# Kernel tuning notes

Measured on AMD Instinct MI355X. Metric: run time of the kernel, lower is better.

The kernel has to match this reference:

```python
import jax, jax.numpy as jnp
import numpy as np

HID = 2048
N_HEADS = 16
N_KV = 16
HEAD_DIM = HID // N_HEADS
N_EXP = 8
TOP_K = 2
MOE_I = 1408
SH_I = 5632
EPS = 1e-6
ROPE_THETA = 1e6


def _rms(x, w):
    v = jnp.mean(jnp.square(x), axis=-1, keepdims=True)
    return (x * jax.lax.rsqrt(v + EPS)) * w


def _rope(q, k):
    # q, k: [B, S, H, D]
    S, D = q.shape[1], q.shape[-1]
    inv = 1.0 / (ROPE_THETA ** (jnp.arange(0, D, 2, dtype=jnp.float32) / D))
    freqs = jnp.arange(S, dtype=jnp.float32)[:, None] * inv[None, :]   # [S, D/2]
    emb = jnp.concatenate([freqs, freqs], axis=-1)                      # [S, D]
    cos = jnp.cos(emb)[None, :, None, :]
    sin = jnp.sin(emb)[None, :, None, :]
    def rot(t):
        t1, t2 = t[..., : D // 2], t[..., D // 2:]
        return jnp.concatenate([-t2, t1], axis=-1)
    return q * cos + rot(q) * sin, k * cos + rot(k) * sin


def setup_inputs() -> dict:
    key = jax.random.key(0)
    ks = jax.random.split(key, 20)
    s = 0.02
    d = {
        "x": jax.random.normal(ks[0], (2, 1024, HID), jnp.float32),
        "w_ln1": jnp.ones((HID,), jnp.float32),
        "wq": jax.random.normal(ks[1], (HID, N_HEADS * HEAD_DIM), jnp.float32) * s,
        "bq": jnp.zeros((N_HEADS * HEAD_DIM,), jnp.float32),
        "wk": jax.random.normal(ks[2], (HID, N_KV * HEAD_DIM), jnp.float32) * s,
        "bk": jnp.zeros((N_KV * HEAD_DIM,), jnp.float32),
        "wv": jax.random.normal(ks[3], (HID, N_KV * HEAD_DIM), jnp.float32) * s,
        "bv": jnp.zeros((N_KV * HEAD_DIM,), jnp.float32),
        "wo": jax.random.normal(ks[4], (N_HEADS * HEAD_DIM, HID), jnp.float32) * s,
        "w_ln2": jnp.ones((HID,), jnp.float32),
        "w_router": jax.random.normal(ks[5], (HID, N_EXP), jnp.float32) * s,
        "w_gate_e": jax.random.normal(ks[6], (N_EXP, HID, MOE_I), jnp.float32) * s,
        "w_up_e": jax.random.normal(ks[7], (N_EXP, HID, MOE_I), jnp.float32) * s,
        "w_down_e": jax.random.normal(ks[8], (N_EXP, MOE_I, HID), jnp.float32) * s,
        "w_sh_gate": jax.random.normal(ks[9], (HID, SH_I), jnp.float32) * s,
        "w_sh_up": jax.random.normal(ks[10], (HID, SH_I), jnp.float32) * s,
        "w_sh_down": jax.random.normal(ks[11], (SH_I, HID), jnp.float32) * s,
        "w_sh_eg": jax.random.normal(ks[12], (HID, 1), jnp.float32) * s,
    }
    return d


def reference(x, w_ln1, wq, bq, wk, bk, wv, bv, wo, w_ln2, w_router,
              w_gate_e, w_up_e, w_down_e, w_sh_gate, w_sh_up, w_sh_down, w_sh_eg):
    B, S, H = x.shape
    # ---- self-attention (pre-norm) ----
    h = _rms(x, w_ln1)
    q = (h @ wq + bq).reshape(B, S, N_HEADS, HEAD_DIM)
    k = (h @ wk + bk).reshape(B, S, N_KV, HEAD_DIM)
    v = (h @ wv + bv).reshape(B, S, N_KV, HEAD_DIM)
    q, k = _rope(q, k)
    rep = N_HEADS // N_KV
    if rep > 1:
        k = jnp.repeat(k, rep, axis=2)
        v = jnp.repeat(v, rep, axis=2)
    scores = jnp.einsum("bqhd,bkhd->bhqk", q, k) * (HEAD_DIM ** -0.5)
    causal = jnp.tril(jnp.ones((S, S), bool))
    scores = jnp.where(causal[None, None], scores, jnp.finfo(scores.dtype).min)
    attn = jax.nn.softmax(scores, axis=-1)
    ctx = jnp.einsum("bhqk,bkhd->bqhd", attn, v).reshape(B, S, N_HEADS * HEAD_DIM)
    x = x + ctx @ wo

    # ---- sparse MoE FFN (pre-norm) ----
    h = _rms(x, w_ln2).reshape(B * S, H)                     # [T, H]
    logits = h @ w_router                                     # [T, E]
    probs = jax.nn.softmax(logits, axis=-1)
    top_w, top_i = jax.lax.top_k(probs, TOP_K)               # norm_topk_prob=False
    combine = jnp.sum(jax.nn.one_hot(top_i, N_EXP, dtype=h.dtype)
                      * top_w[..., None], axis=1)            # [T, E]
    # dense per-expert compute combined with routing weights (same math as
    # the sorted grouped-GEMM dispatch in Qwen2MoeMLPStack)
    g = jnp.einsum("th,ehi->eti", h, w_gate_e)               # [E, T, I]
    u = jnp.einsum("th,ehi->eti", h, w_up_e)
    y = jnp.einsum("eti,eih->eth", jax.nn.silu(g) * u, w_down_e)
    routed = jnp.einsum("eth,te->th", y, combine)            # [T, H]
    # shared expert with sigmoid gate
    sh = (jax.nn.silu(h @ w_sh_gate) * (h @ w_sh_up)) @ w_sh_down
    sh = sh * jax.nn.sigmoid(h @ w_sh_eg)
    x = x + (routed + sh).reshape(B, S, H)
    return x
```

## Files before the change

### kernel.cpp

```cpp
#include <hip/hip_runtime.h>
#include <hip/hip_bf16.h>
#include <math.h>

#define TOKENS 2048
#define HIDDEN 2048
#define NH 16
#define HD 128
#define SEQ 1024
#define MOE_I 1408
#define SH_I 5632
#define K3 6144
#define MAXROWS 5120

typedef __hip_bfloat16 bf16;
typedef short bf16x8 __attribute__((ext_vector_type(8)));
typedef short bf16x4 __attribute__((ext_vector_type(4)));
typedef float f32x4 __attribute__((ext_vector_type(4)));
typedef float f32x16 __attribute__((ext_vector_type(16)));

__device__ __forceinline__ float b2f(bf16 x) { return __bfloat162float(x); }
__device__ __forceinline__ bf16 f2b(float x) { return __float2bfloat16(x); }
__device__ __forceinline__ void split2(float v, short& hi, short& lo) {
    bf16 h = f2b(v);
    bf16 l = f2b(v - b2f(h));
    hi = __builtin_bit_cast(short, h); lo = __builtin_bit_cast(short, l);
}

__device__ __forceinline__ void load_lds16(const void* g, void* l) {
    __builtin_amdgcn_global_load_lds(
        (const __attribute__((address_space(1))) unsigned int*)g,
        (__attribute__((address_space(3))) unsigned int*)l, 16, 0, 0);
}

__global__ __launch_bounds__(256) void rmsnorm3_k(
    const float* __restrict__ x, const float* __restrict__ w, bf16* __restrict__ out)
{
    const int row = blockIdx.x, tid = threadIdx.x;
    const float4* xr = (const float4*)(x + (size_t)row * HIDDEN);
    float4 v1 = xr[tid], v2 = xr[tid + 256];
    float ss = v1.x*v1.x + v1.y*v1.y + v1.z*v1.z + v1.w*v1.w
             + v2.x*v2.x + v2.y*v2.y + v2.z*v2.z + v2.w*v2.w;
    #pragma unroll
    for (int off = 1; off < 64; off <<= 1) ss += __shfl_xor(ss, off);
    __shared__ float ps[4];
    if ((tid & 63) == 0) ps[tid >> 6] = ss;
    __syncthreads();
    float tot = ps[0] + ps[1] + ps[2] + ps[3];
    float r = rsqrtf(tot * (1.0f / HIDDEN) + 1e-6f);
    bf16* o = out + (size_t)row * 4096;
    float vv[8] = {v1.x, v1.y, v1.z, v1.w, v2.x, v2.y, v2.z, v2.w};
    int idx[8]  = {tid*4, tid*4+1, tid*4+2, tid*4+3,
                   1024+tid*4, 1024+tid*4+1, 1024+tid*4+2, 1024+tid*4+3};
    #pragma unroll
    for (int u = 0; u < 8; u++) {
        short hi, lo; split2(vv[u] * r * w[idx[u]], hi, lo);
        o[idx[u]]        = __builtin_bit_cast(bf16, hi);
        o[2048 + idx[u]] = __builtin_bit_cast(bf16, lo);
    }
}

__global__ __launch_bounds__(256) void transpose_wz(
    const float* __restrict__ W, bf16* __restrict__ Wt, int K, int N,
    int nOff, long zsrc, long zdst)
{
    __shared__ float t[32][33];
    W  += (size_t)blockIdx.z * zsrc;
    Wt += (size_t)blockIdx.z * zdst;
    const int n0 = blockIdx.x * 32, k0 = blockIdx.y * 32;
    const int tx = threadIdx.x & 31, ty = threadIdx.x >> 5;
    #pragma unroll
    for (int i = 0; i < 4; i++)
        t[ty + i*8][tx] = W[(size_t)(k0 + ty + i*8) * N + n0 + tx];
    __syncthreads();
    #pragma unroll
    for (int i = 0; i < 4; i++)
        Wt[(size_t)(nOff + n0 + ty + i*8) * K + k0 + tx] = f2b(t[tx][ty + i*8]);
}

__global__ __launch_bounds__(256) void transpose_w3(
    const float* __restrict__ W, bf16* __restrict__ Wt2, int K, int N, int nOff)
{
    __shared__ float t[32][33];
    const int n0 = blockIdx.x * 32, k0 = blockIdx.y * 32;
    const int tx = threadIdx.x & 31, ty = threadIdx.x >> 5;
    #pragma unroll
    for (int i = 0; i < 4; i++)
        t[ty + i*8][tx] = W[(size_t)(k0 + ty + i*8) * N + n0 + tx];
    __syncthreads();
    #pragma unroll
    for (int i = 0; i < 4; i++) {
        float v = t[tx][ty + i*8];
        short hi, lo; split2(v, hi, lo);
        bf16* o = Wt2 + (size_t)(nOff + n0 + ty + i*8) * (2*K) + k0 + tx;
        o[0] = __builtin_bit_cast(bf16, hi);
        o[K] = __builtin_bit_cast(bf16, lo);
    }
}

__global__ __launch_bounds__(256) void gemm_bt(
    const bf16* __restrict__ A, const bf16* __restrict__ Bt,
    float* __restrict__ Cf, bf16* __restrict__ Cb, const float* __restrict__ bias,
    int M, int N, int K, int ldA, int ldB, int ldC, long zCstride, int limb3, int epi)
{
    __shared__ __align__(16) bf16 As[128 * 64];
    __shared__ __align__(16) bf16 Bs[128 * 64];
    const int tid = threadIdx.x;
    const int lane = tid & 63, wid = tid >> 6;
    const int l32 = lane & 31, lh2 = lane >> 5;
    const int wr = wid >> 1, wc = wid & 1;
    int lid = blockIdx.y * gridDim.x + blockIdx.x;
    {
        const int nwg = gridDim.x * gridDim.y;
        const int q = nwg >> 3, r = nwg & 7;
        const int xcd = lid & 7, idx = lid >> 3;
        lid = (xcd < r ? xcd * (q + 1) : r * (q + 1) + (xcd - r) * q) + idx;
    }
    const int m0 = (lid % gridDim.x) * 128, n0 = (lid / gridDim.x) * 128;
    const int koff = blockIdx.z * K;

    int srow[4], sslot[4];
    #pragma unroll
    for (int i = 0; i < 4; i++) {
        const int c = tid + 256*i;
        srow[i]  = c >> 3;
        sslot[i] = (((c & 7) ^ (srow[i] & 7)) << 3);
    }

    f32x16 acc[2][2];
    #pragma unroll
    for (int m = 0; m < 2; m++)
        #pragma unroll
        for (int n = 0; n < 2; n++)
            #pragma unroll
            for (int j = 0; j < 16; j++) acc[m][n][j] = 0.f;

    for (int k0 = 0; k0 < K; k0 += 64) {
        const int kcat = koff + k0;
        int ka = kcat, kb = kcat;
        if (limb3) {
            ka = (kcat >= 4096) ? kcat - 4096 : kcat;
            kb = (kcat >= 2048) ? kcat - 2048 : kcat;
        }
        __syncthreads();
        #pragma unroll
        for (int i = 0; i < 4; i++) {
            load_lds16(A  + (size_t)(m0 + srow[i]) * ldA + ka + sslot[i], As + (tid + 256*i) * 8);
            load_lds16(Bt + (size_t)(n0 + srow[i]) * ldB + kb + sslot[i], Bs + (tid + 256*i) * 8);
        }
        __syncthreads();
        bf16x8 a[2][4], b[2][4];
        #pragma unroll
        for (int m = 0; m < 2; m++) {
            const int r = wr*64 + m*32 + l32, rx = r & 7;
            #pragma unroll
            for (int kk = 0; kk < 4; kk++)
                a[m][kk] = *(const bf16x8*)&As[r*64 + ((((kk<<1)|lh2) ^ rx) << 3)];
        }
        #pragma unroll
        for (int n = 0; n < 2; n++) {
            const int r = wc*64 + n*32 + l32, rx = r & 7;
            #pragma unroll
            for (int kk = 0; kk < 4; kk++)
                b[n][kk] = *(const bf16x8*)&Bs[r*64 + ((((kk<<1)|lh2) ^ rx) << 3)];
        }
        #pragma unroll
        for (int kk = 0; kk < 4; kk++)
            #pragma unroll
            for (int m = 0; m < 2; m++)
                #pragma unroll
                for (int n = 0; n < 2; n++)
                    acc[m][n] = __builtin_amdgcn_mfma_f32_32x32x16_bf16(a[m][kk], b[n][kk], acc[m][n], 0, 0, 0);
    }

    float* Cz = Cf + (size_t)blockIdx.z * zCstride;
    #pragma unroll
    for (int m = 0; m < 2; m++) {
        const int base_m = m0 + wr*64 + m*32 + 4*lh2;
        #pragma unroll
        for (int n = 0; n < 2; n++) {
// ... 148 lines not shown
        #pragma unroll
        for (int n = 0; n < 2; n++) {
            const int r = wc*64 + n*32 + l32, rx = r & 7;
            #pragma unroll
            for (int kk = 0; kk < 4; kk++)
                b[n][kk] = *(const bf16x8*)&Bs[r*64 + ((((kk<<1)|lh2) ^ rx) << 3)];
        }
        #pragma unroll
        for (int kk = 0; kk < 4; kk++)
            #pragma unroll
            for (int m = 0; m < 2; m++)
                #pragma unroll
                for (int n = 0; n < 2; n++)
                    acc[m][n] = __builtin_amdgcn_mfma_f32_32x32x16_bf16(a[m][kk], b[n][kk], acc[m][n], 0, 0, 0);
    }

    #pragma unroll
    for (int m = 0; m < 2; m++) {
        const int base_m = m0 + wr*64 + m*32 + 4*lh2;
        #pragma unroll
        for (int n = 0; n < 2; n++) {
            const int gcol = n0 + wc*64 + n*32 + l32;
            #pragma unroll
            for (int reg = 0; reg < 16; reg++) {
                const int grow = base_m + (reg & 3) + 8*(reg >> 2);
                Y[(size_t)(off + grow) * 2048 + gcol] = f2b(acc[m][n][reg]);
            }
        }
    }
}

__global__ void rope_table_k(float2* __restrict__ cs)
{
    const int i = blockIdx.x * 256 + threadIdx.x;
    const int s = i >> 6, d = i & 63;
    const float fr = (float)s * powf(1.0e6f, -(float)d * (1.0f / 64.0f));
    float c, sn;
    sincosf(fr, &sn, &c);
    cs[i] = make_float2(c, sn);
}

__global__ void rope_f32_k(float* __restrict__ qkv, const float2* __restrict__ cs)
{
    const int idx = blockIdx.x * 256 + threadIdx.x;
    const int d  = idx & 63;
    const int hh = (idx >> 6) & 15;
    const size_t base = (size_t)(idx >> 10) * 6144 + hh * HD;
    const int s = (idx >> 10) & 1023;
    const float2 t = cs[(s << 6) | d];
    const float c = t.x, sn = t.y;
    float q0 = qkv[base + d], q1 = qkv[base + d + 64];
    qkv[base + d]      = q0 * c - q1 * sn;
    qkv[base + d + 64] = q1 * c + q0 * sn;
    float k0 = qkv[base + 2048 + d], k1 = qkv[base + 2048 + d + 64];
    qkv[base + 2048 + d]      = k0 * c - k1 * sn;
    qkv[base + 2048 + d + 64] = k1 * c + k0 * sn;
}

__global__ __launch_bounds__(256) void transpose_v3_k(
    const float* __restrict__ qkv, bf16* __restrict__ vth, bf16* __restrict__ vtl)
{
    __shared__ float t[32][33];
    const int s0 = blockIdx.x * 32, d0 = blockIdx.y * 32;
    const int bh = blockIdx.z, b = bh >> 4, h = bh & 15;
    const int tx = threadIdx.x & 31, ty = threadIdx.x >> 5;
    const float* vb = qkv + ((size_t)b * SEQ) * 6144 + 4096 + h * HD;
    #pragma unroll
    for (int i = 0; i < 4; i++)
        t[ty + i*8][tx] = vb[(size_t)(s0 + ty + i*8) * 6144 + d0 + tx];
    __syncthreads();
    const size_t ob = ((size_t)bh * HD) * SEQ;
    #pragma unroll
    for (int i = 0; i < 4; i++) {
        float val = t[tx][ty + i*8];
        short hi, lo; split2(val, hi, lo);
        const size_t o = ob + (size_t)(d0 + ty + i*8) * SEQ + s0 + tx;
        vth[o] = __builtin_bit_cast(bf16, hi);
        vtl[o] = __builtin_bit_cast(bf16, lo);
    }
}

__global__ __launch_bounds__(256) void attn3_k(
    const float* __restrict__ qkv,
    const bf16* __restrict__ vth, const bf16* __restrict__ vtl,
    bf16* __restrict__ ctx2)
{
    __shared__ __align__(16) bf16 Ksh[32 * 128], Ksl[32 * 128];
    __shared__ __align__(16) bf16 Vth[128 * 32], Vtl[128 * 32];
    __shared__ __align__(16) bf16 Ph[4][16 * 32], Pl[4][16 * 32];
    const int tid = threadIdx.x, lane = tid & 63, wid = tid >> 6;
    const int l16 = lane & 15, lh = lane >> 4;
    const int bh = blockIdx.y, b = bh >> 4, h = bh & 15;
    const int qbase = blockIdx.x * 64;
    const int qw = qbase + wid * 16;
    const float* qp = qkv + ((size_t)b * SEQ) * 6144 + h * HD;
    const float* kp = qkv + ((size_t)b * SEQ) * 6144 + 2048 + h * HD;
    const bf16* vph = vth + ((size_t)bh * HD) * SEQ;
    const bf16* vpl = vtl + ((size_t)bh * HD) * SEQ;

    bf16x8 aqh[4], aql[4];
    #pragma unroll
    for (int c = 0; c < 4; c++) {
        const float* qrow = qp + (size_t)(qw + l16) * 6144 + c*32 + lh*8;
        #pragma unroll
        for (int u = 0; u < 8; u++) {
            short hi, lo; split2(qrow[u], hi, lo);
            aqh[c][u] = hi; aql[c][u] = lo;
        }
    }

    f32x4 o[8];
    #pragma unroll
    for (int n = 0; n < 8; n++) o[n] = (f32x4){0.f, 0.f, 0.f, 0.f};
    float mj[4], lj[4];
    #pragma unroll
    for (int j = 0; j < 4; j++) { mj[j] = -1e30f; lj[j] = 0.f; }

    const int f = tid * 8;
    const int kr = tid >> 3, kc = (tid & 7) * 16;
    const int kt_end = qbase / 32 + 2;
    for (int kt = 0; kt < kt_end; ++kt) {
        const int kv0 = kt * 32;
        __syncthreads();
        {
            const float* krow = kp + (size_t)(kv0 + kr) * 6144 + kc;
            #pragma unroll
            for (int u = 0; u < 4; u++) {
                float4 kv4 = *(const float4*)(krow + u*4);
                short h0, l0, h1, l1, h2s, l2s, h3, l3;
                split2(kv4.x, h0, l0); split2(kv4.y, h1, l1);
                split2(kv4.z, h2s, l2s); split2(kv4.w, h3, l3);
                bf16x4 h4, l4;
                h4[0] = h0; h4[1] = h1; h4[2] = h2s; h4[3] = h3;
                l4[0] = l0; l4[1] = l1; l4[2] = l2s; l4[3] = l3;
                *(bf16x4*)&Ksh[kr*128 + kc + u*4] = h4;
                *(bf16x4*)&Ksl[kr*128 + kc + u*4] = l4;
            }
        }
        load_lds16(vph + (size_t)(f >> 5) * SEQ + kv0 + (f & 31), Vth + f);
        load_lds16(vph + (size_t)((f >> 5) + 64) * SEQ + kv0 + (f & 31), Vth + f + 2048);
        load_lds16(vpl + (size_t)(f >> 5) * SEQ + kv0 + (f & 31), Vtl + f);
        load_lds16(vpl + (size_t)((f >> 5) + 64) * SEQ + kv0 + (f & 31), Vtl + f + 2048);
        __syncthreads();

        f32x4 s0a = (f32x4){0.f,0.f,0.f,0.f}, s1a = (f32x4){0.f,0.f,0.f,0.f};
        #pragma unroll
        for (int c = 0; c < 4; c++) {
            bf16x8 bk0h = *(const bf16x8*)&Ksh[(l16) * 128 + c*32 + lh*8];
            bf16x8 bk0l = *(const bf16x8*)&Ksl[(l16) * 128 + c*32 + lh*8];
            bf16x8 bk1h = *(const bf16x8*)&Ksh[(l16 + 16) * 128 + c*32 + lh*8];
            bf16x8 bk1l = *(const bf16x8*)&Ksl[(l16 + 16) * 128 + c*32 + lh*8];
            s0a = __builtin_amdgcn_mfma_f32_16x16x32_bf16(aqh[c], bk0h, s0a, 0, 0, 0);
            s0a = __builtin_amdgcn_mfma_f32_16x16x32_bf16(aql[c], bk0h, s0a, 0, 0, 0);
            s0a = __builtin_amdgcn_mfma_f32_16x16x32_bf16(aqh[c], bk0l, s0a, 0, 0, 0);
            s1a = __builtin_amdgcn_mfma_f32_16x16x32_bf16(aqh[c], bk1h, s1a, 0, 0, 0);
            s1a = __builtin_amdgcn_mfma_f32_16x16x32_bf16(aql[c], bk1h, s1a, 0, 0, 0);
            s1a = __builtin_amdgcn_mfma_f32_16x16x32_bf16(aqh[c], bk1l, s1a, 0, 0, 0);
        }
        const float scale = 0.08838834764831845f;
        #pragma unroll
        for (int j = 0; j < 4; j++) {
            const int qrow = qw + lh*4 + j;
            float s0 = s0a[j] * scale, s1 = s1a[j] * scale;
            if (kv0 + l16 > qrow)      s0 = -1e30f;
            if (kv0 + l16 + 16 > qrow) s1 = -1e30f;
            float mx = fmaxf(s0, s1);
            #pragma unroll
            for (int off = 1; off < 16; off <<= 1) mx = fmaxf(mx, __shfl_xor(mx, off, 16));
            const float nm = fmaxf(mj[j], mx);
            const float al = __expf(mj[j] - nm);
            const float p0 = __expf(s0 - nm), p1 = __expf(s1 - nm);
            float rs = p0 + p1;
            #pragma unroll
            for (int off = 1; off < 16; off <<= 1) rs += __shfl_xor(rs, off, 16);
            lj[j] = lj[j] * al + rs;
            mj[j] = nm;
            #pragma unroll
            for (int n = 0; n < 8; n++) o[n][j] *= al;
            short h0, l0, h1, l1;
            split2(p0, h0, l0); split2(p1, h1, l1);
            Ph[wid][(lh*4 + j) * 32 + l16]      = __builtin_bit_cast(bf16, h0);
            Pl[wid][(lh*4 + j) * 32 + l16]      = __builtin_bit_cast(bf16, l0);
            Ph[wid][(lh*4 + j) * 32 + l16 + 16] = __builtin_bit_cast(bf16, h1);
            Pl[wid][(lh*4 + j) * 32 + l16 + 16] = __builtin_bit_cast(bf16, l1);
        }
        __syncthreads();
        const bf16x8 aph = *(const bf16x8*)&Ph[wid][l16 * 32 + lh*8];
        const bf16x8 apl = *(const bf16x8*)&Pl[wid][l16 * 32 + lh*8];
        #pragma unroll
        for (int n = 0; n < 8; n++) {
            bf16x8 bvh = *(const bf16x8*)&Vth[(n*16 + l16) * 32 + lh*8];
            bf16x8 bvl = *(const bf16x8*)&Vtl[(n*16 + l16) * 32 + lh*8];
            o[n] = __builtin_amdgcn_mfma_f32_16x16x32_bf16(aph, bvh, o[n], 0, 0, 0);
            o[n] = __builtin_amdgcn_mfma_f32_16x16x32_bf16(apl, bvh, o[n], 0, 0, 0);
            o[n] = __builtin_amdgcn_mfma_f32_16x16x32_bf16(aph, bvl, o[n], 0, 0, 0);
        }
    }

    float inv[4];
    #pragma unroll
    for (int j = 0; j < 4; j++) inv[j] = 1.0f / lj[j];
    #pragma unroll
    for (int n = 0; n < 8; n++)
        #pragma unroll
        for (int j = 0; j < 4; j++) {
            const float v = o[n][j] * inv[j];
            short hi, lo; split2(v, hi, lo);
            const size_t base = ((size_t)b * SEQ + (qw + lh*4 + j)) * 4096 + h * HD + n*16 + l16;
            ctx2[base]        = __builtin_bit_cast(bf16, hi);
            ctx2[base + 2048] = __builtin_bit_cast(bf16, lo);
        }
}

__global__ __launch_bounds__(256) void combine_rms_k(
    const float* __restrict__ x, const float* __restrict__ xp,
    const float* __restrict__ w, float* __restrict__ x1, bf16* __restrict__ h2)
{
    const int row = blockIdx.x, tid = threadIdx.x;
    const size_t rb = (size_t)row * HIDDEN;
    const long zs = (long)TOKENS * HIDDEN;
    float4 v[2];
    #pragma unroll
    for (int u = 0; u < 2; u++) {
        const int i = tid + u * 256;
        float4 a  = ((const float4*)(x + rb))[i];
        float4 p0 = ((const float4*)(xp + rb))[i];
        float4 p1 = ((const float4*)(xp + zs + rb))[i];
        float4 p2 = ((const float4*)(xp + 2*zs + rb))[i];
        v[u].x = a.x + p0.x + p1.x + p2.x;
        v[u].y = a.y + p0.y + p1.y + p2.y;
        v[u].z = a.z + p0.z + p1.z + p2.z;
        v[u].w = a.w + p0.w + p1.w + p2.w;
        ((float4*)(x1 + rb))[i] = v[u];
    }
    float ss = v[0].x*v[0].x + v[0].y*v[0].y + v[0].z*v[0].z + v[0].w*v[0].w
             + v[1].x*v[1].x + v[1].y*v[1].y + v[1].z*v[1].z + v[1].w*v[1].w;
    #pragma unroll
    for (int off = 1; off < 64; off <<= 1) ss += __shfl_xor(ss, off);
    __shared__ float ps[4];
    if ((tid & 63) == 0) ps[tid >> 6] = ss;
    __syncthreads();
    float tot = ps[0] + ps[1] + ps[2] + ps[3];
    float r = rsqrtf(tot * (1.0f / HIDDEN) + 1e-6f);
    #pragma unroll
    for (int u = 0; u < 2; u++) {
        const int i = (tid + u * 256) * 4;
        h2[rb + i]     = f2b(v[u].x * r * w[i]);
        h2[rb + i + 1] = f2b(v[u].y * r * w[i+1]);
        h2[rb + i + 2] = f2b(v[u].z * r * w[i+2]);
        h2[rb + i + 3] = f2b(v[u].w * r * w[i+3]);
    }
}

__global__ __launch_bounds__(256) void router_k(
    const float* __restrict__ x1, const float* __restrict__ wln,
    const float* __restrict__ wr, const float* __restrict__ weg,
    float* __restrict__ combine, float* __restrict__ sigeg)
{
    const int wid = threadIdx.x >> 6, lane = threadIdx.x & 63;
    const int t = blockIdx.x * 4 + wid;
    const float* xr = x1 + (size_t)t * HIDDEN;
    float ss = 0.f;
    for (int c = lane; c < HIDDEN; c += 64) { const float v = xr[c]; ss += v * v; }
    #pragma unroll
    for (int off = 1; off < 64; off <<= 1) ss += __shfl_xor(ss, off);
    const float r = rsqrtf(ss * (1.0f / HIDDEN) + 1e-6f);

    float acc[9];
    #pragma unroll
    for (int e = 0; e < 9; e++) acc[e] = 0.f;
    for (int c = lane; c < HIDDEN; c += 64) {
        const float hv = xr[c] * r * wln[c];
        const float* wrow = wr + (size_t)c * 8;
        #pragma unroll
        for (int e = 0; e < 8; e++) acc[e] += hv * wrow[e];
        acc[8] += hv * weg[c];
    }
    #pragma unroll
    for (int e = 0; e < 9; e++)
        #pragma unroll
        for (int off = 1; off < 64; off <<= 1) acc[e] += __shfl_xor(acc[e], off);
    float mx = acc[0];
    #pragma unroll
    for (int e = 1; e < 8; e++) mx = fmaxf(mx, acc[e]);
    float p[8], s = 0.f;
    #pragma unroll
    for (int e = 0; e < 8; e++) { p[e] = expf(acc[e] - mx); s += p[e]; }
    const float invs = 1.0f / s;
    #pragma unroll
    for (int e = 0; e < 8; e++) p[e] *= invs;
    int i1 = 0;
    #pragma unroll
    for (int e = 1; e < 8; e++) if (p[e] > p[i1]) i1 = e;
    int i2 = (i1 == 0) ? 1 : 0;
    #pragma unroll
    for (int e = 0; e < 8; e++) if (e != i1 && p[e] > p[i2]) i2 = e;
    if (lane < 8) combine[(size_t)t * 8 + lane] = (lane == i1 || lane == i2) ? p[lane] : 0.f;
    if (lane == 0) sigeg[t] = 1.0f / (1.0f + expf(-acc[8]));
}

__global__ __launch_bounds__(256) void count_fill_k(
    const float* __restrict__ comb, int* __restrict__ offc, int* __restrict__ perm,
    float* __restrict__ scale, int* __restrict__ inv)
{
    __shared__ int cnt[8], off[9], fil[8];
    const int tid = threadIdx.x;
    if (tid < 8) { cnt[tid] = 0; fil[tid] = 0; }
    __syncthreads();
    for (int t = tid; t < TOKENS; t += 256)
        #pragma unroll
        for (int e = 0; e < 8; e++)
            if (comb[(size_t)t * 8 + e] > 0.f) atomicAdd(&cnt[e], 1);
    __syncthreads();
    if (tid == 0) {
        off[0] = 0;
        for (int e = 0; e < 8; e++) off[e+1] = off[e] + ((cnt[e] + 127) & ~127);
    }
    __syncthreads();
    for (int i = tid; i < MAXROWS; i += 256) { perm[i] = -1; scale[i] = 0.f; }
    __syncthreads();
    for (int t = tid; t < TOKENS; t += 256) {
        int j = 0;
        #pragma unroll
        for (int e = 0; e < 8; e++) {
            const float c = comb[(size_t)t * 8 + e];
            if (c > 0.f) {
                int s = atomicAdd(&fil[e], 1);
                int slot = off[e] + s;
                perm[slot] = t;
                scale[slot] = c;
                inv[t * 2 + j] = slot;
                j++;
            }
        }
    }
    __syncthreads();
    if (tid < 9) offc[8 + tid] = off[tid];
}

__global__ void silu_k(const bf16* __restrict__ g, bf16* __restrict__ a,
                       const float* __restrict__ rowScale,
                       int I, int ldg, int rowsConst, const int* __restrict__ rowsPtr)
{
    const int idx = (blockIdx.x * 256 + threadIdx.x) * 4;
    const int rows = rowsPtr ? *rowsPtr : rowsConst;
    const int row = idx / I;
    if (row >= rows) return;
    const int col = idx - row * I;
    const float s = rowScale[row];
    const bf16* gr = g + (size_t)row * ldg + col;
    bf16* ar = a + (size_t)row * I + col;
    #pragma unroll
    for (int c = 0; c < 4; c++) {
        const float gv = b2f(gr[c]), uv = b2f(gr[I + c]);
        ar[c] = f2b(s * gv / (1.0f + __expf(-gv)) * uv);
    }
}

__global__ void final_k(const float* __restrict__ x1, const bf16* __restrict__ y,
                        const int* __restrict__ inv, const float* __restrict__ ysh,
                        float* __restrict__ out)
{
    const int i = blockIdx.x * 256 + threadIdx.x;
    const int t = i >> 9;
    const int col = (i & 511) * 4;
    const int s0 = inv[t*2], s1 = inv[t*2 + 1];
    const long zs = (long)TOKENS * HIDDEN;
    float4 a  = ((const float4*)x1)[i];
    float4 h0 = ((const float4*)ysh)[i];
    float4 h1 = ((const float4*)(ysh + zs))[i];
    const bf16* y0 = y + (size_t)s0 * 2048 + col;
    const bf16* y1 = y + (size_t)s1 * 2048 + col;
    float4 r;
    r.x = a.x + h0.x + h1.x + b2f(y0[0]) + b2f(y1[0]);
    r.y = a.y + h0.y + h1.y + b2f(y0[1]) + b2f(y1[1]);
    r.z = a.z + h0.z + h1.z + b2f(y0[2]) + b2f(y1[2]);
    r.w = a.w + h0.w + h1.w + b2f(y0[3]) + b2f(y1[3]);
    ((float4*)out)[i] = r;
}

extern "C" void kernel_launch(void* const* d_in, const int* in_sizes, int n_in,
                              void* d_out, int out_size, void* d_ws, size_t ws_size,
                              hipStream_t stream)
{
    const float* x     = (const float*)d_in[0];
    const float* w_ln1 = (const float*)d_in[1];
    const float* wq    = (const float*)d_in[2];
    const float* bq    = (const float*)d_in[3];
    const float* wk    = (const float*)d_in[4];
    const float* bk    = (const float*)d_in[5];
    const float* wv    = (const float*)d_in[6];
    const float* bv    = (const float*)d_in[7];
    const float* wo    = (const float*)d_in[8];
    const float* w_ln2 = (const float*)d_in[9];
    const float* w_rt  = (const float*)d_in[10];
    const float* w_ge  = (const float*)d_in[11];
    const float* w_ue  = (const float*)d_in[12];
    const float* w_de  = (const float*)d_in[13];
    const float* w_sg  = (const float*)d_in[14];
    const float* w_su  = (const float*)d_in[15];
    const float* w_sd  = (const float*)d_in[16];
    const float* w_eg  = (const float*)d_in[17];
    float* out = (float*)d_out;
    (void)in_sizes; (void)n_in; (void)out_size; (void)ws_size;

    char* ws = (char*)d_ws;
    float* x1    = (float*)(ws + 0);
    bf16*  h2    = (bf16*)(ws + 16777216);
    float* comb  = (float*)(ws + 25165824);
    float* seg   = (float*)(ws + 25231360);
    int*   offc  = (int*)(ws + 25239552);
    float* scale = (float*)(ws + 25243648);
    int*   perm  = (int*)(ws + 25276416);
    int*   inv   = (int*)(ws + 25297920);
    float* bqkv  = (float*)(ws + 25314304);
    float2* ropecs = (float2*)(ws + 25338880);
    const size_t S = 25863168;
    bf16*  hcat  = (bf16*)(ws + S);
    bf16*  wtqkv = (bf16*)(ws + S + 16777216);
    float* qkvf  = (float*)(ws + S + 67108864);
    bf16*  vth   = (bf16*)(ws + S);
    bf16*  vtl   = (bf16*)(ws + S + 8388608);
    bf16*  ctx2  = (bf16*)(ws + S + 16777216);
    bf16*  wt3o  = (bf16*)(ws + S + 33554432);
    float* xp    = (float*)(ws + S + 50331648);
    bf16*  wtgu  = (bf16*)(ws + S);
    bf16*  gb    = (bf16*)(ws + S + 92274688);
    bf16*  ab    = (bf16*)(ws + S);
    bf16*  wtd   = (bf16*)(ws + S + 14417920);
    bf16*  ymoe  = (bf16*)(ws + S + 60555264);
    bf16*  wtshgu = (bf16*)(ws + S);
    bf16*  gsh    = (bf16*)(ws + S + 81526784);
    bf16*  ash    = (bf16*)(ws + S);
    bf16*  wtshd  = (bf16*)(ws + S + 23068672);
    float* ysh    = (float*)(ws + S + 81526784);

    rmsnorm3_k<<<TOKENS, 256, 0, stream>>>(x, w_ln1, hcat);
    (void)hipMemcpyAsync(bqkv,        bq, 8192, hipMemcpyDeviceToDevice, stream);
    (void)hipMemcpyAsync(bqkv + 2048, bk, 8192, hipMemcpyDeviceToDevice, stream);
    (void)hipMemcpyAsync(bqkv + 4096, bv, 8192, hipMemcpyDeviceToDevice, stream);
    rope_table_k<<<256, 256, 0, stream>>>(ropecs);

    transpose_w3<<<dim3(64, 64), 256, 0, stream>>>(wq, wtqkv, HIDDEN, HIDDEN, 0);
    transpose_w3<<<dim3(64, 64), 256, 0, stream>>>(wk, wtqkv, HIDDEN, HIDDEN, 2048);
    transpose_w3<<<dim3(64, 64), 256, 0, stream>>>(wv, wtqkv, HIDDEN, HIDDEN, 4096);
    gemm_bt<<<dim3(16, 48, 1), 256, 0, stream>>>(hcat, wtqkv, qkvf, nullptr, bqkv,
                                                 TOKENS, 6144, K3, 4096, 4096, 6144, 0, 1, 5);

    rope_f32_k<<<8192, 256, 0, stream>>>(qkvf, ropecs);
    transpose_v3_k<<<dim3(32, 4, 32), 256, 0, stream>>>(qkvf, vth, vtl);
    attn3_k<<<dim3(16, 32), 256, 0, stream>>>(qkvf, vth, vtl, ctx2);

    transpose_w3<<<dim3(64, 64), 256, 0, stream>>>(wo, wt3o, HIDDEN, HIDDEN, 0);
    gemm_bt<<<dim3(16, 16, 3), 256, 0, stream>>>(ctx2, wt3o, xp, nullptr, nullptr,
                                                 TOKENS, HIDDEN, 2048, 4096, 4096, 2048,
                                                 (long)TOKENS * HIDDEN, 1, 4);
    combine_rms_k<<<TOKENS, 256, 0, stream>>>(x, xp, w_ln2, x1, h2);

    router_k<<<TOKENS / 4, 256, 0, stream>>>(x1, w_ln2, w_rt, w_eg, comb, seg);
    count_fill_k<<<1, 256, 0, stream>>>(comb, offc, perm, scale, inv);

    transpose_wz<<<dim3(44, 64, 8), 256, 0, stream>>>(w_ge, wtgu, HIDDEN, MOE_I, 0,
                                                      (long)HIDDEN*MOE_I, (long)2816*HIDDEN);
    transpose_wz<<<dim3(44, 64, 8), 256, 0, stream>>>(w_ue, wtgu, HIDDEN, MOE_I, MOE_I,
                                                      (long)HIDDEN*MOE_I, (long)2816*HIDDEN);
    gemm_gu<<<dim3(MAXROWS/128, 22, 8), 256, 0, stream>>>(h2, wtgu, offc, perm, gb);
    silu_k<<<(MAXROWS * MOE_I) / 1024, 256, 0, stream>>>(gb, ab, scale, MOE_I, 2816, 0, offc + 16);
    transpose_wz<<<dim3(64, 44, 8), 256, 0, stream>>>(w_de, wtd, MOE_I, HIDDEN, 0,
                                                      (long)MOE_I*HIDDEN, (long)HIDDEN*MOE_I);
    gemm_down<<<dim3(MAXROWS/128, 16, 8), 256, 0, stream>>>(ab, wtd, offc, ymoe);

    transpose_wz<<<dim3(176, 64, 1), 256, 0, stream>>>(w_sg, wtshgu, HIDDEN, SH_I, 0, 0, 0);
    transpose_wz<<<dim3(176, 64, 1), 256, 0, stream>>>(w_su, wtshgu, HIDDEN, SH_I, SH_I, 0, 0);
    gemm_bt<<<dim3(16, 88, 1), 256, 0, stream>>>(h2, wtshgu, nullptr, gsh, nullptr,
                                                 TOKENS, 2*SH_I, HIDDEN, HIDDEN, HIDDEN, 2*SH_I, 0, 0, 0);
    silu_k<<<(TOKENS * SH_I) / 1024, 256, 0, stream>>>(gsh, ash, seg, SH_I, 2*SH_I, TOKENS, nullptr);
    transpose_wz<<<dim3(64, 176, 1), 256, 0, stream>>>(w_sd, wtshd, SH_I, HIDDEN, 0, 0, 0);
    gemm_bt<<<dim3(16, 16, 2), 256, 0, stream>>>(ash, wtshd, ysh, nullptr, nullptr,
                                                 TOKENS, HIDDEN, SH_I/2, SH_I, SH_I, 2048,
                                                 (long)TOKENS * HIDDEN, 0, 4);

    final_k<<<(TOKENS * HIDDEN) / 1024, 256, 0, stream>>>(x1, ymoe, inv, ysh, out);
}
```

Before: 1.025 ms.

## Merge weight transposes, widen attention KV tile with swizzled LDS, fuse router into RMS

Several weight-transpose launches are merged into single kernels that pick their source by blockIdx.z, and the wo transpose moves up front into a non-overlapping workspace slot. The attention kernel now processes 64-key tiles instead of 32, uses XOR-swizzled LDS layouts for K, V and P to avoid bank conflicts, and reuses one shared buffer for K and P. The router's logits and gate are computed inside the combine+RMS kernel, so x1 is not read a second time and a launch is dropped. The risks are higher LDS use (64KB) limiting attention occupancy, and a single thread doing the per-token softmax and top-k.

```diff
diff --git a/kernel.cpp b/kernel.cpp
--- a/kernel.cpp
+++ b/kernel.cpp
@@ -77,24 +77,67 @@
         Wt[(size_t)(nOff + n0 + ty + i*8) * K + k0 + tx] = f2b(t[tx][ty + i*8]);
 }
 
-__global__ __launch_bounds__(256) void transpose_w3(
-    const float* __restrict__ W, bf16* __restrict__ Wt2, int K, int N, int nOff)
-{
+__global__ __launch_bounds__(256) void transpose_qkvo_k(
+    const float* __restrict__ wq, const float* __restrict__ wk,
+    const float* __restrict__ wv, const float* __restrict__ wo,
+    bf16* __restrict__ wtqkv, bf16* __restrict__ wt3o)
+{
+    const int z = blockIdx.z;
+    const float* W = (z == 0) ? wq : (z == 1) ? wk : (z == 2) ? wv : wo;
+    bf16* Wt2 = (z < 3) ? wtqkv : wt3o;
+    const int nOff = (z < 3) ? z * 2048 : 0;
     __shared__ float t[32][33];
     const int n0 = blockIdx.x * 32, k0 = blockIdx.y * 32;
     const int tx = threadIdx.x & 31, ty = threadIdx.x >> 5;
     #pragma unroll
     for (int i = 0; i < 4; i++)
-        t[ty + i*8][tx] = W[(size_t)(k0 + ty + i*8) * N + n0 + tx];
+        t[ty + i*8][tx] = W[(size_t)(k0 + ty + i*8) * 2048 + n0 + tx];
     __syncthreads();
     #pragma unroll
     for (int i = 0; i < 4; i++) {
         float v = t[tx][ty + i*8];
         short hi, lo; split2(v, hi, lo);
-        bf16* o = Wt2 + (size_t)(nOff + n0 + ty + i*8) * (2*K) + k0 + tx;
-        o[0] = __builtin_bit_cast(bf16, hi);
-        o[K] = __builtin_bit_cast(bf16, lo);
-    }
+        bf16* o = Wt2 + (size_t)(nOff + n0 + ty + i*8) * 4096 + k0 + tx;
+        o[0]    = __builtin_bit_cast(bf16, hi);
+        o[2048] = __builtin_bit_cast(bf16, lo);
+    }
+}
+
+__global__ __launch_bounds__(256) void transpose_moegu_k(
+    const float* __restrict__ ge, const float* __restrict__ ue, bf16* __restrict__ wtgu)
+{
+    const int z = blockIdx.z, e = z & 7;
+    const float* W = ((z < 8) ? ge : ue) + (size_t)e * HIDDEN * MOE_I;
+    bf16* Wt = wtgu + (size_t)e * 2816 * HIDDEN;
+    const int nOff = (z < 8) ? 0 : MOE_I;
+    __shared__ float t[32][33];
+    const int n0 = blockIdx.x * 32, k0 = blockIdx.y * 32;
+    const int tx = threadIdx.x & 31, ty = threadIdx.x >> 5;
+    #pragma unroll
+    for (int i = 0; i < 4; i++)
+        t[ty + i*8][tx] = W[(size_t)(k0 + ty + i*8) * MOE_I + n0 + tx];
+    __syncthreads();
+    #pragma unroll
+    for (int i = 0; i < 4; i++)
+        Wt[(size_t)(nOff + n0 + ty + i*8) * HIDDEN + k0 + tx] = f2b(t[tx][ty + i*8]);
+}
+
+__global__ __launch_bounds__(256) void transpose_shgu_k(
+    const float* __restrict__ sg, const float* __restrict__ su, bf16* __restrict__ dst)
+{
+    const int z = blockIdx.z;
+    const float* W = z ? su : sg;
+    const int nOff = z * SH_I;
+    __shared__ float t[32][33];
+    const int n0 = blockIdx.x * 32, k0 = blockIdx.y * 32;
+    const int tx = threadIdx.x & 31, ty = threadIdx.x >> 5;
+    #pragma unroll
+    for (int i = 0; i < 4; i++)
+        t[ty + i*8][tx] = W[(size_t)(k0 + ty + i*8) * SH_I + n0 + tx];
+    __syncthreads();
+    #pragma unroll
+    for (int i = 0; i < 4; i++)
+        dst[(size_t)(nOff + n0 + ty + i*8) * HIDDEN + k0 + tx] = f2b(t[tx][ty + i*8]);
 }
 
 __global__ __launch_bounds__(256) void gemm_bt(
@@ -409,12 +452,17 @@
 
 __global__ __launch_bounds__(256) void attn3_k(
     const float* __restrict__ qkv,
-    const bf16* __restrict__ vth, const bf16* __restrict__ vtl,
+    const bf16* __restrict__ vthg, const bf16* __restrict__ vtlg,
     bf16* __restrict__ ctx2)
 {
-    __shared__ __align__(16) bf16 Ksh[32 * 128], Ksl[32 * 128];
-    __shared__ __align__(16) bf16 Vth[128 * 32], Vtl[128 * 32];
-    __shared__ __align__(16) bf16 Ph[4][16 * 32], Pl[4][16 * 32];
+    __shared__ __align__(16) bf16 SM[32768];
+    bf16* Ksh = SM;
+    bf16* Ksl = SM + 8192;
+    bf16* Vth = SM + 16384;
+    bf16* Vtl = SM + 24576;
+    bf16* Ph  = SM;
+    bf16* Pl  = SM + 4096;
+
     const int tid = threadIdx.x, lane = tid & 63, wid = tid >> 6;
     const int l16 = lane & 15, lh = lane >> 4;
     const int bh = blockIdx.y, b = bh >> 4, h = bh & 15;
@@ -422,8 +470,8 @@
     const int qw = qbase + wid * 16;
     const float* qp = qkv + ((size_t)b * SEQ) * 6144 + h * HD;
     const float* kp = qkv + ((size_t)b * SEQ) * 6144 + 2048 + h * HD;
-    const bf16* vph = vth + ((size_t)bh * HD) * SEQ;
-    const bf16* vpl = vtl + ((size_t)bh * HD) * SEQ;
+    const bf16* vph = vthg + ((size_t)bh * HD) * SEQ;
+    const bf16* vpl = vtlg + ((size_t)bh * HD) * SEQ;
 
     bf16x8 aqh[4], aql[4];
     #pragma unroll
@@ -443,16 +491,17 @@
     #pragma unroll
     for (int j = 0; j < 4; j++) { mj[j] = -1e30f; lj[j] = 0.f; }
 
-    const int f = tid * 8;
-    const int kr = tid >> 3, kc = (tid & 7) * 16;
-    const int kt_end = qbase / 32 + 2;
+    const int kr = tid >> 2;
+    const int kc = (tid & 3) * 32;
+    const int krx = kr & 15;
+    const int kt_end = blockIdx.x + 1;
     for (int kt = 0; kt < kt_end; ++kt) {
-        const int kv0 = kt * 32;
+        const int kv0 = kt * 64;
         __syncthreads();
         {
             const float* krow = kp + (size_t)(kv0 + kr) * 6144 + kc;
             #pragma unroll
-            for (int u = 0; u < 4; u++) {
+            for (int u = 0; u < 8; u++) {
                 float4 kv4 = *(const float4*)(krow + u*4);
                 short h0, l0, h1, l1, h2s, l2s, h3, l3;
                 split2(kv4.x, h0, l0); split2(kv4.y, h1, l1);
@@ -460,67 +509,88 @@
                 bf16x4 h4, l4;
                 h4[0] = h0; h4[1] = h1; h4[2] = h2s; h4[3] = h3;
                 l4[0] = l0; l4[1] = l1; l4[2] = l2s; l4[3] = l3;
-                *(bf16x4*)&Ksh[kr*128 + kc + u*4] = h4;
-                *(bf16x4*)&Ksl[kr*128 + kc + u*4] = l4;
+                const int s = (((kc + u*4) >> 3) ^ krx);
+                const int dst = kr*128 + (s << 3) + ((u & 1) * 4);
+                *(bf16x4*)&Ksh[dst] = h4;
+                *(bf16x4*)&Ksl[dst] = l4;
             }
         }
-        load_lds16(vph + (size_t)(f >> 5) * SEQ + kv0 + (f & 31), Vth + f);
-        load_lds16(vph + (size_t)((f >> 5) + 64) * SEQ + kv0 + (f & 31), Vth + f + 2048);
-        load_lds16(vpl + (size_t)(f >> 5) * SEQ + kv0 + (f & 31), Vtl + f);
-        load_lds16(vpl + (size_t)((f >> 5) + 64) * SEQ + kv0 + (f & 31), Vtl + f + 2048);
+        #pragma unroll
+        for (int i = 0; i < 4; i++) {
+            const int c = tid + 256*i;
+            const int row = c >> 3, sl = (c & 7) ^ (row & 7);
+            load_lds16(vph + (size_t)row * SEQ + kv0 + (sl << 3), Vth + c*8);
+            load_lds16(vpl + (size_t)row * SEQ + kv0 + (sl << 3), Vtl + c*8);
+        }
         __syncthreads();
 
-        f32x4 s0a = (f32x4){0.f,0.f,0.f,0.f}, s1a = (f32x4){0.f,0.f,0.f,0.f};
+        f32x4 sg[4];
+        #pragma unroll
+        for (int g = 0; g < 4; g++) sg[g] = (f32x4){0.f,0.f,0.f,0.f};
         #pragma unroll
         for (int c = 0; c < 4; c++) {
-            bf16x8 bk0h = *(const bf16x8*)&Ksh[(l16) * 128 + c*32 + lh*8];
-            bf16x8 bk0l = *(const bf16x8*)&Ksl[(l16) * 128 + c*32 + lh*8];
-            bf16x8 bk1h = *(const bf16x8*)&Ksh[(l16 + 16) * 128 + c*32 + lh*8];
-            bf16x8 bk1l = *(const bf16x8*)&Ksl[(l16 + 16) * 128 + c*32 + lh*8];
-            s0a = __builtin_amdgcn_mfma_f32_16x16x32_bf16(aqh[c], bk0h, s0a, 0, 0, 0);
-            s0a = __builtin_amdgcn_mfma_f32_16x16x32_bf16(aql[c], bk0h, s0a, 0, 0, 0);
-            s0a = __builtin_amdgcn_mfma_f32_16x16x32_bf16(aqh[c], bk0l, s0a, 0, 0, 0);
-            s1a = __builtin_amdgcn_mfma_f32_16x16x32_bf16(aqh[c], bk1h, s1a, 0, 0, 0);
-            s1a = __builtin_amdgcn_mfma_f32_16x16x32_bf16(aql[c], bk1h, s1a, 0, 0, 0);
-            s1a = __builtin_amdgcn_mfma_f32_16x16x32_bf16(aqh[c], bk1l, s1a, 0, 0, 0);
-        }
+            #pragma unroll
+            for (int g = 0; g < 4; g++) {
+                const int row = l16 + g*16;
+                const int sl = (((c*4 + lh) ^ (row & 15)) << 3);
+                bf16x8 bkh = *(const bf16x8*)&Ksh[row*128 + sl];
+                bf16x8 bkl = *(const bf16x8*)&Ksl[row*128 + sl];
+                sg[g] = __builtin_amdgcn_mfma_f32_16x16x32_bf16(aqh[c], bkh, sg[g], 0, 0, 0);
+                sg[g] = __builtin_amdgcn_mfma_f32_16x16x32_bf16(aql[c], bkh, sg[g], 0, 0, 0);
+                sg[g] = __builtin_amdgcn_mfma_f32_16x16x32_bf16(aqh[c], bkl, sg[g], 0, 0, 0);
+            }
+        }
+        __syncthreads();
+
         const float scale = 0.08838834764831845f;
         #pragma unroll
         for (int j = 0; j < 4; j++) {
             const int qrow = qw + lh*4 + j;
-            float s0 = s0a[j] * scale, s1 = s1a[j] * scale;
-            if (kv0 + l16 > qrow)      s0 = -1e30f;
-            if (kv0 + l16 + 16 > qrow) s1 = -1e30f;
-            float mx = fmaxf(s0, s1);
+            float sv[4];
+            #pragma unroll
+            for (int g = 0; g < 4; g++) {
+                sv[g] = sg[g][j] * scale;
+                if (kv0 + l16 + g*16 > qrow) sv[g] = -1e30f;
+            }
+            float mx = fmaxf(fmaxf(sv[0], sv[1]), fmaxf(sv[2], sv[3]));
             #pragma unroll
             for (int off = 1; off < 16; off <<= 1) mx = fmaxf(mx, __shfl_xor(mx, off, 16));
             const float nm = fmaxf(mj[j], mx);
             const float al = __expf(mj[j] - nm);
-            const float p0 = __expf(s0 - nm), p1 = __expf(s1 - nm);
-            float rs = p0 + p1;
+            float pg[4], rs = 0.f;
+            #pragma unroll
+            for (int g = 0; g < 4; g++) { pg[g] = __expf(sv[g] - nm); rs += pg[g]; }
             #pragma unroll
             for (int off = 1; off < 16; off <<= 1) rs += __shfl_xor(rs, off, 16);
             lj[j] = lj[j] * al + rs;
             mj[j] = nm;
             #pragma unroll
             for (int n = 0; n < 8; n++) o[n][j] *= al;
-            short h0, l0, h1, l1;
-            split2(p0, h0, l0); split2(p1, h1, l1);
-            Ph[wid][(lh*4 + j) * 32 + l16]      = __builtin_bit_cast(bf16, h0);
-            Pl[wid][(lh*4 + j) * 32 + l16]      = __builtin_bit_cast(bf16, l0);
-            Ph[wid][(lh*4 + j) * 32 + l16 + 16] = __builtin_bit_cast(bf16, h1);
-            Pl[wid][(lh*4 + j) * 32 + l16 + 16] = __builtin_bit_cast(bf16, l1);
-        }
-        __syncthreads();
-        const bf16x8 aph = *(const bf16x8*)&Ph[wid][l16 * 32 + lh*8];
-        const bf16x8 apl = *(const bf16x8*)&Pl[wid][l16 * 32 + lh*8];
-        #pragma unroll
-        for (int n = 0; n < 8; n++) {
-            bf16x8 bvh = *(const bf16x8*)&Vth[(n*16 + l16) * 32 + lh*8];
-            bf16x8 bvl = *(const bf16x8*)&Vtl[(n*16 + l16) * 32 + lh*8];
-            o[n] = __builtin_amdgcn_mfma_f32_16x16x32_bf16(aph, bvh, o[n], 0, 0, 0);
-            o[n] = __builtin_amdgcn_mfma_f32_16x16x32_bf16(apl, bvh, o[n], 0, 0, 0);
-            o[n] = __builtin_amdgcn_mfma_f32_16x16x32_bf16(aph, bvl, o[n], 0, 0, 0);
+            const int prow = lh*4 + j;
+            #pragma unroll
+            for (int g = 0; g < 4; g++) {
+                short hi, lo; split2(pg[g], hi, lo);
+                const int col = l16 + g*16;
+                const int addr = wid*1024 + prow*64 + ((((col >> 3) ^ (prow & 7)) << 3)) + (col & 7);
+                Ph[addr] = __builtin_bit_cast(bf16, hi);
+                Pl[addr] = __builtin_bit_cast(bf16, lo);
+            }
+        }
+        #pragma unroll
+        for (int ks = 0; ks < 2; ks++) {
+            const int psl = (((ks*4 + lh) ^ (l16 & 7)) << 3);
+            bf16x8 aph = *(const bf16x8*)&Ph[wid*1024 + l16*64 + psl];
+            bf16x8 apl = *(const bf16x8*)&Pl[wid*1024 + l16*64 + psl];
+            #pragma unroll
+            for (int n = 0; n < 8; n++) {
+                const int row = n*16 + l16;
+                const int vsl = (((ks*4 + lh) ^ (row & 7)) << 3);
+                bf16x8 bvh = *(const bf16x8*)&Vth[row*64 + vsl];
+                bf16x8 bvl = *(const bf16x8*)&Vtl[row*64 + vsl];
+                o[n] = __builtin_amdgcn_mfma_f32_16x16x32_bf16(aph, bvh, o[n], 0, 0, 0);
+                o[n] = __builtin_amdgcn_mfma_f32_16x16x32_bf16(apl, bvh, o[n], 0, 0, 0);
+                o[n] = __builtin_amdgcn_mfma_f32_16x16x32_bf16(aph, bvl, o[n], 0, 0, 0);
+            }
         }
     }
 
@@ -539,13 +609,18 @@
         }
 }
 
-__global__ __launch_bounds__(256) void combine_rms_k(
+__global__ __launch_bounds__(256) void combine_rms_router_k(
     const float* __restrict__ x, const float* __restrict__ xp,
-    const float* __restrict__ w, float* __restrict__ x1, bf16* __restrict__ h2)
+    const float* __restrict__ wln, const float* __restrict__ wr,
+    const float* __restrict__ weg,
+    float* __restrict__ x1, bf16* __restrict__ h2,
+    float* __restrict__ comb, float* __restrict__ sigeg)
 {
     const int row = blockIdx.x, tid = threadIdx.x;
     const size_t rb = (size_t)row * HIDDEN;
     const long zs = (long)TOKENS * HIDDEN;
+    __shared__ float ps[4];
+    __shared__ float pacc[4][9];
     float4 v[2];
     #pragma unroll
     for (int u = 0; u < 2; u++) {
@@ -564,66 +639,60 @@
              + v[1].x*v[1].x + v[1].y*v[1].y + v[1].z*v[1].z + v[1].w*v[1].w;
     #pragma unroll
     for (int off = 1; off < 64; off <<= 1) ss += __shfl_xor(ss, off);
-    __shared__ float ps[4];
     if ((tid & 63) == 0) ps[tid >> 6] = ss;
     __syncthreads();
-    float tot = ps[0] + ps[1] + ps[2] + ps[3];
-    float r = rsqrtf(tot * (1.0f / HIDDEN) + 1e-6f);
+    const float tot = ps[0] + ps[1] + ps[2] + ps[3];
+    const float r = rsqrtf(tot * (1.0f / HIDDEN) + 1e-6f);
+
+    float acc[9];
+    #pragma unroll
+    for (int e = 0; e < 9; e++) acc[e] = 0.f;
     #pragma unroll
     for (int u = 0; u < 2; u++) {
         const int i = (tid + u * 256) * 4;
-        h2[rb + i]     = f2b(v[u].x * r * w[i]);
-        h2[rb + i + 1] = f2b(v[u].y * r * w[i+1]);
-        h2[rb + i + 2] = f2b(v[u].z * r * w[i+2]);
-        h2[rb + i + 3] = f2b(v[u].w * r * w[i+3]);
-    }
-}
-
-__global__ __launch_bounds__(256) void router_k(
-    const float* __restrict__ x1, const float* __restrict__ wln,
-    const float* __restrict__ wr, const float* __restrict__ weg,
-    float* __restrict__ combine, float* __restrict__ sigeg)
-{
-    const int wid = threadIdx.x >> 6, lane = threadIdx.x & 63;
-    const int t = blockIdx.x * 4 + wid;
-    const float* xr = x1 + (size_t)t * HIDDEN;
-    float ss = 0.f;
-    for (int c = lane; c < HIDDEN; c += 64) { const float v = xr[c]; ss += v * v; }
-    #pragma unroll
-    for (int off = 1; off < 64; off <<= 1) ss += __shfl_xor(ss, off);
-    const float r = rsqrtf(ss * (1.0f / HIDDEN) + 1e-6f);
-
-    float acc[9];
-    #pragma unroll
-    for (int e = 0; e < 9; e++) acc[e] = 0.f;
-    for (int c = lane; c < HIDDEN; c += 64) {
-        const float hv = xr[c] * r * wln[c];
-        const float* wrow = wr + (size_t)c * 8;
-        #pragma unroll
-        for (int e = 0; e < 8; e++) acc[e] += hv * wrow[e];
-        acc[8] += hv * weg[c];
+        const float vv[4] = {v[u].x, v[u].y, v[u].z, v[u].w};
+        #pragma unroll
+        for (int q = 0; q < 4; q++) {
+            const float hv = vv[q] * r * wln[i + q];
+            h2[rb + i + q] = f2b(hv);
+            const float* wrow = wr + (size_t)(i + q) * 8;
+            #pragma unroll
+            for (int e = 0; e < 8; e++) acc[e] += hv * wrow[e];
+            acc[8] += hv * weg[i + q];
+        }
     }
     #pragma unroll
     for (int e = 0; e < 9; e++)
         #pragma unroll
         for (int off = 1; off < 64; off <<= 1) acc[e] += __shfl_xor(acc[e], off);
-    float mx = acc[0];
-    #pragma unroll
-    for (int e = 1; e < 8; e++) mx = fmaxf(mx, acc[e]);
-    float p[8], s = 0.f;
-    #pragma unroll
-    for (int e = 0; e < 8; e++) { p[e] = expf(acc[e] - mx); s += p[e]; }
-    const float invs = 1.0f / s;
-    #pragma unroll
-    for (int e = 0; e < 8; e++) p[e] *= invs;
-    int i1 = 0;
-    #pragma unroll
-    for (int e = 1; e < 8; e++) if (p[e] > p[i1]) i1 = e;
-    int i2 = (i1 == 0) ? 1 : 0;
-    #pragma unroll
-    for (int e = 0; e < 8; e++) if (e != i1 && p[e] > p[i2]) i2 = e;
-    if (lane < 8) combine[(size_t)t * 8 + lane] = (lane == i1 || lane == i2) ? p[lane] : 0.f;
-    if (lane == 0) sigeg[t] = 1.0f / (1.0f + expf(-acc[8]));
+    if ((tid & 63) == 0)
+        #pragma unroll
+        for (int e = 0; e < 9; e++) pacc[tid >> 6][e] = acc[e];
+    __syncthreads();
+    if (tid == 0) {
+        float lg[9];
+        #pragma unroll
+        for (int e = 0; e < 9; e++) lg[e] = pacc[0][e] + pacc[1][e] + pacc[2][e] + pacc[3][e];
+        float mx = lg[0];
+        #pragma unroll
+        for (int e = 1; e < 8; e++) mx = fmaxf(mx, lg[e]);
+        float p[8], s = 0.f;
+        #pragma unroll
+        for (int e = 0; e < 8; e++) { p[e] = expf(lg[e] - mx); s += p[e]; }
+        const float invs = 1.0f / s;
+        #pragma unroll
+        for (int e = 0; e < 8; e++) p[e] *= invs;
+        int i1 = 0;
+        #pragma unroll
+        for (int e = 1; e < 8; e++) if (p[e] > p[i1]) i1 = e;
+        int i2 = (i1 == 0) ? 1 : 0;
+        #pragma unroll
+        for (int e = 0; e < 8; e++) if (e != i1 && p[e] > p[i2]) i2 = e;
+        #pragma unroll
+        for (int e = 0; e < 8; e++)
+            comb[(size_t)row * 8 + e] = (e == i1 || e == i2) ? p[e] : 0.f;
+        sigeg[row] = 1.0f / (1.0f + expf(-lg[8]));
+    }
 }
 
 __global__ __launch_bounds__(256) void count_fill_k(
@@ -746,10 +815,10 @@
     bf16*  hcat  = (bf16*)(ws + S);
     bf16*  wtqkv = (bf16*)(ws + S + 16777216);
     float* qkvf  = (float*)(ws + S + 67108864);
+    bf16*  wt3o  = (bf16*)(ws + S + 117440512);
     bf16*  vth   = (bf16*)(ws + S);
     bf16*  vtl   = (bf16*)(ws + S + 8388608);
     bf16*  ctx2  = (bf16*)(ws + S + 16777216);
-    bf16*  wt3o  = (bf16*)(ws + S + 33554432);
     float* xp    = (float*)(ws + S + 50331648);
     bf16*  wtgu  = (bf16*)(ws + S);
     bf16*  gb    = (bf16*)(ws + S + 92274688);
@@ -768,9 +837,7 @@
     (void)hipMemcpyAsync(bqkv + 4096, bv, 8192, hipMemcpyDeviceToDevice, stream);
     rope_table_k<<<256, 256, 0, stream>>>(ropecs);
 
-    transpose_w3<<<dim3(64, 64), 256, 0, stream>>>(wq, wtqkv, HIDDEN, HIDDEN, 0);
-    transpose_w3<<<dim3(64, 64), 256, 0, stream>>>(wk, wtqkv, HIDDEN, HIDDEN, 2048);
-    transpose_w3<<<dim3(64, 64), 256, 0, stream>>>(wv, wtqkv, HIDDEN, HIDDEN, 4096);
+    transpose_qkvo_k<<<dim3(64, 64, 4), 256, 0, stream>>>(wq, wk, wv, wo, wtqkv, wt3o);
     gemm_bt<<<dim3(16, 48, 1), 256, 0, stream>>>(hcat, wtqkv, qkvf, nullptr, bqkv,
                                                  TOKENS, 6144, K3, 4096, 4096, 6144, 0, 1, 5);
 
@@ -778,27 +845,21 @@
     transpose_v3_k<<<dim3(32, 4, 32), 256, 0, stream>>>(qkvf, vth, vtl);
     attn3_k<<<dim3(16, 32), 256, 0, stream>>>(qkvf, vth, vtl, ctx2);
 
-    transpose_w3<<<dim3(64, 64), 256, 0, stream>>>(wo, wt3o, HIDDEN, HIDDEN, 0);
     gemm_bt<<<dim3(16, 16, 3), 256, 0, stream>>>(ctx2, wt3o, xp, nullptr, nullptr,
                                                  TOKENS, HIDDEN, 2048, 4096, 4096, 2048,
                                                  (long)TOKENS * HIDDEN, 1, 4);
-    combine_rms_k<<<TOKENS, 256, 0, stream>>>(x, xp, w_ln2, x1, h2);
-
-    router_k<<<TOKENS / 4, 256, 0, stream>>>(x1, w_ln2, w_rt, w_eg, comb, seg);
+    combine_rms_router_k<<<TOKENS, 256, 0, stream>>>(x, xp, w_ln2, w_rt, w_eg,
+                                                     x1, h2, comb, seg);
     count_fill_k<<<1, 256, 0, stream>>>(comb, offc, perm, scale, inv);
 
-    transpose_wz<<<dim3(44, 64, 8), 256, 0, stream>>>(w_ge, wtgu, HIDDEN, MOE_I, 0,
-                                                      (long)HIDDEN*MOE_I, (long)2816*HIDDEN);
-    transpose_wz<<<dim3(44, 64, 8), 256, 0, stream>>>(w_ue, wtgu, HIDDEN, MOE_I, MOE_I,
-                                                      (long)HIDDEN*MOE_I, (long)2816*HIDDEN);
+    transpose_moegu_k<<<dim3(44, 64, 16), 256, 0, stream>>>(w_ge, w_ue, wtgu);
     gemm_gu<<<dim3(MAXROWS/128, 22, 8), 256, 0, stream>>>(h2, wtgu, offc, perm, gb);
     silu_k<<<(MAXROWS * MOE_I) / 1024, 256, 0, stream>>>(gb, ab, scale, MOE_I, 2816, 0, offc + 16);
     transpose_wz<<<dim3(64, 44, 8), 256, 0, stream>>>(w_de, wtd, MOE_I, HIDDEN, 0,
                                                       (long)MOE_I*HIDDEN, (long)HIDDEN*MOE_I);
     gemm_down<<<dim3(MAXROWS/128, 16, 8), 256, 0, stream>>>(ab, wtd, offc, ymoe);
 
-    transpose_wz<<<dim3(176, 64, 1), 256, 0, stream>>>(w_sg, wtshgu, HIDDEN, SH_I, 0, 0, 0);
-    transpose_wz<<<dim3(176, 64, 1), 256, 0, stream>>>(w_su, wtshgu, HIDDEN, SH_I, SH_I, 0, 0);
+    transpose_shgu_k<<<dim3(176, 64, 2), 256, 0, stream>>>(w_sg, w_su, wtshgu);
     gemm_bt<<<dim3(16, 88, 1), 256, 0, stream>>>(h2, wtshgu, nullptr, gsh, nullptr,
                                                  TOKENS, 2*SH_I, HIDDEN, HIDDEN, HIDDEN, 2*SH_I, 0, 0, 0);
     silu_k<<<(TOKENS * SH_I) / 1024, 256, 0, stream>>>(gsh, ash, seg, SH_I, 2*SH_I, TOKENS, nullptr);
```

New measurement: 971.6 us. 1.05x faster.
